# Kernel optimization log

Hardware: AMD Instinct MI355X
Metric: run time of the kernel (lower is better)

The kernel has to match this reference:

```python
import jax, jax.numpy as jnp
import numpy as np

N_NODES = 100000
N_EDGES = 3200000
IN_DIM, HID_DIM, OUT_DIM = 256, 128, 64


def setup_inputs() -> dict:
    key = jax.random.key(0)
    ks = jax.random.split(key, 8)
    x = jax.random.normal(ks[0], (N_NODES, IN_DIM), dtype=jnp.float32)
    edge_index = jax.random.randint(ks[1], (2, N_EDGES), 0, N_NODES, dtype=jnp.int64)
    s = 0.05
    return {
        "x": x,
        "edge_index": edge_index,
        "W1": jax.random.normal(ks[2], (IN_DIM, HID_DIM), dtype=jnp.float32) * s,
        "b1": jnp.zeros((HID_DIM,), dtype=jnp.float32),
        "W2": jax.random.normal(ks[3], (HID_DIM, HID_DIM), dtype=jnp.float32) * s,
        "b2": jnp.zeros((HID_DIM,), dtype=jnp.float32),
        "W3": jax.random.normal(ks[4], (HID_DIM, OUT_DIM), dtype=jnp.float32) * s,
        "b3": jnp.zeros((OUT_DIM,), dtype=jnp.float32),
    }


def _gcn_conv(x, src, dst, deg_inv_sqrt, W, b):
    """PyG GCNConv: D^-1/2 (A+I) D^-1/2 (X W) + b.
    src/dst already include self-loops; deg_inv_sqrt precomputed per node."""
    h = x @ W  # [N, F_out] - transform first (smaller message dim)
    norm = deg_inv_sqrt[src] * deg_inv_sqrt[dst]  # [E]
    msg = h[src] * norm[:, None]  # gather + scale
    out = jax.ops.segment_sum(msg, dst, num_segments=x.shape[0])  # scatter-add
    return out + b


def reference(x, edge_index, W1, b1, W2, b2, W3, b3):
    n = x.shape[0]
    loops = jnp.arange(n, dtype=edge_index.dtype)
    src = jnp.concatenate([edge_index[0], loops])
    dst = jnp.concatenate([edge_index[1], loops])
    # symmetric normalization degree over (A + I), counted on dst as in PyG
    deg = jax.ops.segment_sum(jnp.ones_like(dst, dtype=x.dtype), dst, num_segments=n)
    deg_inv_sqrt = jnp.where(deg > 0, jax.lax.rsqrt(deg), 0.0)

    h = _gcn_conv(x, src, dst, deg_inv_sqrt, W1, b1)
    h = jax.nn.relu(h)  # dropout in eval mode = identity
    h = _gcn_conv(h, src, dst, deg_inv_sqrt, W2, b2)
    h = jax.nn.relu(h)
    h = _gcn_conv(h, src, dst, deg_inv_sqrt, W3, b3)
    return h
```

## Files before the change

### kernel.cpp

```cpp
#include <hip/hip_runtime.h>
#include <hip/hip_fp16.h>

constexpr int IN_DIM  = 256;
constexpr int HID_DIM = 128;
constexpr int OUT_DIM = 64;

constexpr int NPB_SHIFT = 8;
constexpr int NPB   = 1 << NPB_SHIFT;
constexpr int NBMAX = 512;
constexpr int CHUNK = 4096;
constexpr int CAP_B = 12288;

typedef _Float16 half8 __attribute__((ext_vector_type(8)));
typedef float floatx4 __attribute__((ext_vector_type(4)));


__global__ __launch_bounds__(256) void k_hist(const int* __restrict__ dst, int E, int NB,
                                              int* __restrict__ bsize) {
  __shared__ int h[NBMAX];
  for (int i = threadIdx.x; i < NB; i += 256) h[i] = 0;
  __syncthreads();
  int e0 = blockIdx.x * CHUNK;
  int e1 = min(e0 + CHUNK, E);
  for (int e = e0 + threadIdx.x; e < e1; e += 256) {
    int d = __builtin_nontemporal_load(&dst[e]);
    atomicAdd(&h[d >> NPB_SHIFT], 1);
  }
  __syncthreads();
  for (int b = threadIdx.x; b < NB; b += 256) {
    int c = h[b];
    if (c) atomicAdd(&bsize[b], c);
  }
}

__global__ __launch_bounds__(512) void k_scanb(const int* __restrict__ bsize, int NB, int E,
                                               int* __restrict__ boff, int* __restrict__ gcur) {
  __shared__ int sh[NBMAX + 1];
  for (int i = threadIdx.x; i < NB; i += 512) sh[i] = bsize[i];
  __syncthreads();
  if (threadIdx.x == 0) {
    int run = 0;
    for (int b = 0; b < NB; b++) { int v = sh[b]; sh[b] = run; run += v; }
    sh[NB] = run;
  }
  __syncthreads();
  for (int i = threadIdx.x; i < NB; i += 512) { boff[i] = sh[i]; gcur[i] = sh[i]; }
  if (threadIdx.x == 0) boff[NB] = sh[NB];
}

__global__ __launch_bounds__(256) void k_binA(const int* __restrict__ src,
                                              const int* __restrict__ dst, int E, int NB,
                                              int* __restrict__ gcur,
                                              unsigned int* __restrict__ bin) {
  __shared__ unsigned int sbuf[CHUNK];
  __shared__ unsigned short sbb[CHUNK];
  __shared__ int h[NBMAX], lofs[NBMAX], wofs[NBMAX], hcur[NBMAX];
  for (int i = threadIdx.x; i < NB; i += 256) h[i] = 0;
  __syncthreads();
  int e0 = blockIdx.x * CHUNK;
  int e1 = min(e0 + CHUNK, E);
  for (int e = e0 + threadIdx.x; e < e1; e += 256) {
    int d = __builtin_nontemporal_load(&dst[e]);
    atomicAdd(&h[d >> NPB_SHIFT], 1);
  }
  __syncthreads();
  for (int b = threadIdx.x; b < NB; b += 256) {
    int c = h[b];
    if (c) wofs[b] = atomicAdd(&gcur[b], c);
  }
  if (threadIdx.x == 0) {
    int run = 0;
    for (int b = 0; b < NB; b++) { lofs[b] = run; run += h[b]; }
  }
  __syncthreads();
  for (int b = threadIdx.x; b < NB; b += 256) hcur[b] = lofs[b];
  __syncthreads();
  for (int e = e0 + threadIdx.x; e < e1; e += 256) {
    int d = dst[e];
    int s = src[e];
    int b = d >> NPB_SHIFT;
    int p = atomicAdd(&hcur[b], 1);
    sbuf[p] = ((unsigned int)(d & (NPB - 1)) << 24) | (unsigned int)s;
    sbb[p] = (unsigned short)b;
  }
  __syncthreads();
  int total = e1 - e0;
  for (int i = threadIdx.x; i < total; i += 256) {
    int b = sbb[i];
    bin[(size_t)wofs[b] + (i - lofs[b])] = sbuf[i];
  }
}

__global__ __launch_bounds__(256) void k_passB(const unsigned int* __restrict__ bin,
                                               const int* __restrict__ boff, int NB, int N, int E,
                                               int* __restrict__ rowptr, float* __restrict__ dis,
                                               int* __restrict__ col) {
  __shared__ unsigned int colbuf[CAP_B];
  __shared__ int lcnt[NPB], lofs2[NPB + 1], lpos[NPB];
  int b = blockIdx.x;
  int lo = b << NPB_SHIFT;
  int e0 = boff[b], e1 = boff[b + 1];
  int tot = e1 - e0;
  if (threadIdx.x < NPB) lcnt[threadIdx.x] = 0;
  __syncthreads();
  for (int i = threadIdx.x; i < tot; i += 256) {
    unsigned int v = bin[(size_t)e0 + i];
    atomicAdd(&lcnt[v >> 24], 1);
  }
  __syncthreads();
  if (threadIdx.x == 0) {
    int run = 0;
    for (int i = 0; i < NPB; i++) { lofs2[i] = run; run += lcnt[i]; }
    lofs2[NPB] = run;
  }
  __syncthreads();
  if (threadIdx.x < NPB) {
    int node = lo + threadIdx.x;
    if (node < N) {
      rowptr[node] = e0 + lofs2[threadIdx.x];
      dis[node] = rsqrtf((float)lcnt[threadIdx.x] + 1.0f);
    }
    lpos[threadIdx.x] = lofs2[threadIdx.x];
  }
  __syncthreads();
  for (int i = threadIdx.x; i < tot; i += 256) {
    unsigned int v = bin[(size_t)e0 + i];
    int idx = v >> 24;
    int p = atomicAdd(&lpos[idx], 1);
    unsigned int s = v & 0x00FFFFFFu;
    if (p < CAP_B) colbuf[p] = s;
    else col[(size_t)e0 + p] = (int)s;
  }
  __syncthreads();
  int cp = min(tot, CAP_B);
  for (int i = threadIdx.x; i < cp; i += 256)
    __builtin_nontemporal_store(colbuf[i], (unsigned int*)&col[(size_t)e0 + i]);
  if (b == 0 && threadIdx.x == 0) rowptr[N] = E;
}


template <int K, int N>
__device__ inline void packW_one(const float* __restrict__ W, _Float16* __restrict__ Wp,
                                 int idx) {
  int k = idx / N, n = idx % N;
  int ct = n >> 4, ks = k >> 5, q = (k >> 3) & 3, j = k & 7;
  int lane = (n & 15) + (q << 4);
  Wp[((((size_t)ct * (K / 32) + ks) * 64 + lane) << 3) + j] = (_Float16)W[idx];
}

__global__ __launch_bounds__(256) void k_packAll(const float* __restrict__ W1, _Float16* __restrict__ Wp1,
                                                 const float* __restrict__ W2, _Float16* __restrict__ Wp2,
                                                 const float* __restrict__ W3, _Float16* __restrict__ Wp3) {
  constexpr int S1 = IN_DIM * HID_DIM;
  constexpr int S2 = S1 + HID_DIM * HID_DIM;
  constexpr int S3 = S2 + HID_DIM * OUT_DIM;
  int idx = blockIdx.x * 256 + threadIdx.x;
  if (idx < S1) packW_one<IN_DIM, HID_DIM>(W1, Wp1, idx);
  else if (idx < S2) packW_one<HID_DIM, HID_DIM>(W2, Wp2, idx - S1);
  else if (idx < S3) packW_one<HID_DIM, OUT_DIM>(W3, Wp3, idx - S2);
}


template <int K, int N, typename AT>
__global__ __launch_bounds__(256) void k_gemm_mfma(const AT* __restrict__ A,
                                                   const _Float16* __restrict__ Wp,
                                                   const float* __restrict__ dis,
                                                   __half* __restrict__ out, int M) {
  constexpr int CT = N / 16;
  constexpr int KS = K / 32;
  constexpr int KH = (K * N * 2 > 32768) ? 2 : 1;
  constexpr int KSH = KS / KH;
  constexpr int NF4 = CT * KSH * 64;
  __shared__ float4 wlds[NF4];

  const int wave = threadIdx.x >> 6, lane = threadIdx.x & 63;
  const int q = lane >> 4, mlane = lane & 15;
  const int row0 = blockIdx.x * 64 + wave * 16;
  int arow = row0 + mlane;
  if (arow > M - 1) arow = M - 1;

  const float4* __restrict__ wsrc = (const float4*)Wp;

  floatx4 acc[CT];
#pragma unroll
  for (int c = 0; c < CT; c++) acc[c] = (floatx4){0.f, 0.f, 0.f, 0.f};

#pragma unroll
  for (int h = 0; h < KH; h++) {
    if (h) __syncthreads();
#pragma unroll
    for (int i = threadIdx.x; i < NF4; i += 256) {
      int c = i / (KSH * 64);
      int rem = i & (KSH * 64 - 1);
      wlds[i] = wsrc[(size_t)(c * KS + h * KSH) * 64 + rem];
    }
    __syncthreads();

#pragma unroll
    for (int ksl = 0; ksl < KSH; ksl++) {
      const int ks = h * KSH + ksl;
      half8 a;
      if constexpr (sizeof(AT) == 4) {
        const float* ap = &A[(size_t)arow * K + ks * 32 + q * 8];
        float4 f0 = *(const float4*)ap;
        float4 f1 = *(const float4*)(ap + 4);
        a[0] = (_Float16)f0.x; a[1] = (_Float16)f0.y;
        a[2] = (_Float16)f0.z; a[3] = (_Float16)f0.w;
        a[4] = (_Float16)f1.x; a[5] = (_Float16)f1.y;
        a[6] = (_Float16)f1.z; a[7] = (_Float16)f1.w;
      } else {
        a = *(const half8*)&A[(size_t)arow * K + ks * 32 + q * 8];
      }
#pragma unroll
      for (int c = 0; c < CT; c++) {
        half8 b = *(const half8*)&wlds[(c * KSH + ksl) * 64 + lane];
        acc[c] = __builtin_amdgcn_mfma_f32_16x16x32_f16(a, b, acc[c], 0, 0, 0);
      }
    }
  }

  float dv[4]; int orow[4];
#pragma unroll
  for (int r = 0; r < 4; r++) {
    orow[r] = row0 + q * 4 + r;
    dv[r] = (orow[r] < M) ? dis[orow[r]] : 0.f;
  }
#pragma unroll
  for (int c = 0; c < CT; c++) {
    int cl = c * 16 + mlane;
#pragma unroll
    for (int r = 0; r < 4; r++)
      if (orow[r] < M)
        out[(size_t)orow[r] * N + cl] = __float2half_rn(dv[r] * acc[c][r]);
  }
}


template <bool RELU>
__global__ __launch_bounds__(256) void k_agg128(const __half* __restrict__ g,
                                                const int* __restrict__ rowptr,
                                                const int* __restrict__ col,
                                                const float* __restrict__ dis,
                                                const float* __restrict__ bias,
                                                __half* __restrict__ out, int n) {
  const int lane = threadIdx.x & 63;
  const int r = lane >> 4;
  const int c = lane & 15;
  const int v = blockIdx.x * 4 + (threadIdx.x >> 6);
  if (v >= n) return;
  int p = rowptr[v], end = rowptr[v + 1];
  const float dv = dis[v];

  float acc[8];
#pragma unroll
  for (int i = 0; i < 8; i++) acc[i] = 0.f;
  if (r == 0) {
    half8 s = *(const half8*)&g[(size_t)v * 128 + c * 8];
#pragma unroll
    for (int i = 0; i < 8; i++) acc[i] += (float)s[i];
  }

  int rem = end - p;
  while (rem >= 8) {
    int u0 = __builtin_nontemporal_load(&col[p + r]);
    int u1 = __builtin_nontemporal_load(&col[p + 4 + r]);
    half8 t0 = *(const half8*)&g[(size_t)u0 * 128 + c * 8];
    half8 t1 = *(const half8*)&g[(size_t)u1 * 128 + c * 8];
#pragma unroll
    for (int i = 0; i < 8; i++) acc[i] += (float)t0[i];
#pragma unroll
    for (int i = 0; i < 8; i++) acc[i] += (float)t1[i];
    p += 8; rem -= 8;
  }
  if (rem >= 4) {
    int u0 = __builtin_nontemporal_load(&col[p + r]);
    half8 t0 = *(const half8*)&g[(size_t)u0 * 128 + c * 8];
#pragma unroll
    for (int i = 0; i < 8; i++) acc[i] += (float)t0[i];
    p += 4; rem -= 4;
  }
  if (rem > 0) {
    int rr = (r < rem) ? r : 0;
    int u0 = __builtin_nontemporal_load(&col[p + rr]);
    half8 t0 = *(const half8*)&g[(size_t)u0 * 128 + c * 8];
    float m = (r < rem) ? 1.f : 0.f;
#pragma unroll
    for (int i = 0; i < 8; i++) acc[i] = fmaf(m, (float)t0[i], acc[i]);
  }

#pragma unroll
  for (int i = 0; i < 8; i++) {
    acc[i] += __shfl_xor(acc[i], 16);
    acc[i] += __shfl_xor(acc[i], 32);
  }

  if (r == 0) {
    half8 h;
#pragma unroll
    for (int i = 0; i < 8; i++) {
      float o = fmaf(dv, acc[i], bias[c * 8 + i]);
      if (RELU) o = fmaxf(o, 0.f);
      h[i] = (_Float16)o;
    }
    *(half8*)&out[(size_t)v * 128 + c * 8] = h;
  }
}


__global__ __launch_bounds__(256) void k_agg64(const __half* __restrict__ g,
                                               const int* __restrict__ rowptr,
                                               const int* __restrict__ col,
                                               const float* __restrict__ dis,
                                               const float* __restrict__ bias,
                                               float* __restrict__ out, int n) {
  const int lane = threadIdx.x & 63;
  const int r = lane >> 3;
  const int c = lane & 7;
  const int v = blockIdx.x * 4 + (threadIdx.x >> 6);
  if (v >= n) return;
  int p = rowptr[v], end = rowptr[v + 1];
  const float dv = dis[v];

  float acc[8];
#pragma unroll
  for (int i = 0; i < 8; i++) acc[i] = 0.f;
  if (r == 0) {
    half8 s = *(const half8*)&g[(size_t)v * 64 + c * 8];
#pragma unroll
    for (int i = 0; i < 8; i++) acc[i] += (float)s[i];
  }

  int rem = end - p;
  while (rem >= 16) {
    int u0 = __builtin_nontemporal_load(&col[p + r]);
    int u1 = __builtin_nontemporal_load(&col[p + 8 + r]);
    half8 t0 = *(const half8*)&g[(size_t)u0 * 64 + c * 8];
    half8 t1 = *(const half8*)&g[(size_t)u1 * 64 + c * 8];
#pragma unroll
    for (int i = 0; i < 8; i++) acc[i] += (float)t0[i];
#pragma unroll
    for (int i = 0; i < 8; i++) acc[i] += (float)t1[i];
    p += 16; rem -= 16;
  }
  if (rem >= 8) {
    int u0 = __builtin_nontemporal_load(&col[p + r]);
    half8 t0 = *(const half8*)&g[(size_t)u0 * 64 + c * 8];
#pragma unroll
    for (int i = 0; i < 8; i++) acc[i] += (float)t0[i];
    p += 8; rem -= 8;
  }
  if (rem > 0) {
    int rr = (r < rem) ? r : 0;
    int u0 = __builtin_nontemporal_load(&col[p + rr]);
    half8 t0 = *(const half8*)&g[(size_t)u0 * 64 + c * 8];
    float m = (r < rem) ? 1.f : 0.f;
#pragma unroll
    for (int i = 0; i < 8; i++) acc[i] = fmaf(m, (float)t0[i], acc[i]);
  }

#pragma unroll
  for (int i = 0; i < 8; i++) {
    acc[i] += __shfl_xor(acc[i], 8);
    acc[i] += __shfl_xor(acc[i], 16);
    acc[i] += __shfl_xor(acc[i], 32);
  }

  if (r == 0) {
    float4 o0, o1;
    float ov[8];
#pragma unroll
    for (int i = 0; i < 8; i++) ov[i] = fmaf(dv, acc[i], bias[c * 8 + i]);
    o0.x = ov[0]; o0.y = ov[1]; o0.z = ov[2]; o0.w = ov[3];
    o1.x = ov[4]; o1.y = ov[5]; o1.z = ov[6]; o1.w = ov[7];
    *(float4*)&out[(size_t)v * 64 + c * 8]     = o0;
    *(float4*)&out[(size_t)v * 64 + c * 8 + 4] = o1;
  }
}


extern "C" void kernel_launch(void* const* d_in, const int* in_sizes, int n_in,
                              void* d_out, int out_size, void* d_ws, size_t ws_size,
                              hipStream_t stream) {
  const float* x  = (const float*)d_in[0];
  const int*   ei = (const int*)d_in[1];
  const float* W1 = (const float*)d_in[2];
  const float* b1 = (const float*)d_in[3];
  const float* W2 = (const float*)d_in[4];
  const float* b2 = (const float*)d_in[5];
  const float* W3 = (const float*)d_in[6];
  const float* b3 = (const float*)d_in[7];
  float* outp = (float*)d_out;

  const int N = in_sizes[0] / IN_DIM;
  const int E = in_sizes[1] / 2;
  const int* src = ei;
  const int* dst = ei + E;
  const int NB = (N + NPB - 1) >> NPB_SHIFT;

  char* w = (char*)d_ws;
  auto take = [&](size_t bytes) {
    char* r = w;
    w += (bytes + 255) & ~size_t(255);
    return r;
  };
  float*  dis    = (float*)take((size_t)N * 4);
  int*    rowptr = (int*)take((size_t)(N + 1) * 4);
  int*    bsize  = (int*)take((size_t)NB * 4);
  int*    boff   = (int*)take((size_t)(NB + 1) * 4);
  int*    gcur   = (int*)take((size_t)NB * 4);
  int*    col    = (int*)take((size_t)E * 4);
  unsigned int* bin = (unsigned int*)take((size_t)E * 4);
  _Float16* Wp1  = (_Float16*)take((size_t)IN_DIM * HID_DIM * 2);
  _Float16* Wp2  = (_Float16*)take((size_t)HID_DIM * HID_DIM * 2);
  _Float16* Wp3  = (_Float16*)take((size_t)HID_DIM * OUT_DIM * 2);
  __half* gbuf   = (__half*)take((size_t)N * 128 * 2);
  __half* bufH   = (__half*)take((size_t)N * 128 * 2);

  const int cb = (E + CHUNK - 1) / CHUNK;
  hipMemsetAsync(bsize, 0, (size_t)NB * 4, stream);
  hipLaunchKernelGGL(k_hist, dim3(cb), dim3(256), 0, stream, dst, E, NB, bsize);
  hipLaunchKernelGGL(k_scanb, dim3(1), dim3(512), 0, stream, bsize, NB, E, boff, gcur);
  hipLaunchKernelGGL(k_binA, dim3(cb), dim3(256), 0, stream, src, dst, E, NB, gcur, bin);
  hipLaunchKernelGGL(k_passB, dim3(NB), dim3(256), 0, stream, bin, boff, NB, N, E, rowptr, dis, col);

  hipLaunchKernelGGL(k_packAll, dim3((IN_DIM * HID_DIM + HID_DIM * HID_DIM + HID_DIM * OUT_DIM + 255) / 256),
                     dim3(256), 0, stream, W1, Wp1, W2, Wp2, W3, Wp3);

  const int gb = (N + 63) / 64;
  const int ab = (N + 3) / 4;
  hipLaunchKernelGGL((k_gemm_mfma<IN_DIM, HID_DIM, float>), dim3(gb), dim3(256), 0, stream, x, Wp1, dis, gbuf, N);
  hipLaunchKernelGGL((k_agg128<true>), dim3(ab), dim3(256), 0, stream, gbuf, rowptr, col, dis, b1, bufH, N);
  hipLaunchKernelGGL((k_gemm_mfma<HID_DIM, HID_DIM, __half>), dim3(gb), dim3(256), 0, stream, bufH, Wp2, dis, gbuf, N);
  hipLaunchKernelGGL((k_agg128<true>), dim3(ab), dim3(256), 0, stream, gbuf, rowptr, col, dis, b2, bufH, N);
  hipLaunchKernelGGL((k_gemm_mfma<HID_DIM, OUT_DIM, __half>), dim3(gb), dim3(256), 0, stream, bufH, Wp3, dis, gbuf, N);
  hipLaunchKernelGGL(k_agg64, dim3(ab), dim3(256), 0, stream, gbuf, rowptr, col, dis, b3, outp, N);
}
```

Before: 614.3 us.

## Batch neighbor index loads via wave shuffles and split 128-dim aggregation launches

```diff
diff --git a/kernel.cpp b/kernel.cpp
--- a/kernel.cpp
+++ b/kernel.cpp
@@ -242,11 +242,11 @@
                                                 const int* __restrict__ col,
                                                 const float* __restrict__ dis,
                                                 const float* __restrict__ bias,
-                                                __half* __restrict__ out, int n) {
+                                                __half* __restrict__ out, int n, int v0) {
   const int lane = threadIdx.x & 63;
   const int r = lane >> 4;
   const int c = lane & 15;
-  const int v = blockIdx.x * 4 + (threadIdx.x >> 6);
+  const int v = v0 + blockIdx.x * 4 + (threadIdx.x >> 6);
   if (v >= n) return;
   int p = rowptr[v], end = rowptr[v + 1];
   const float dv = dis[v];
@@ -260,32 +260,40 @@
     for (int i = 0; i < 8; i++) acc[i] += (float)s[i];
   }
 
-  int rem = end - p;
-  while (rem >= 8) {
-    int u0 = __builtin_nontemporal_load(&col[p + r]);
-    int u1 = __builtin_nontemporal_load(&col[p + 4 + r]);
-    half8 t0 = *(const half8*)&g[(size_t)u0 * 128 + c * 8];
-    half8 t1 = *(const half8*)&g[(size_t)u1 * 128 + c * 8];
-#pragma unroll
-    for (int i = 0; i < 8; i++) acc[i] += (float)t0[i];
-#pragma unroll
-    for (int i = 0; i < 8; i++) acc[i] += (float)t1[i];
-    p += 8; rem -= 8;
-  }
-  if (rem >= 4) {
-    int u0 = __builtin_nontemporal_load(&col[p + r]);
-    half8 t0 = *(const half8*)&g[(size_t)u0 * 128 + c * 8];
-#pragma unroll
-    for (int i = 0; i < 8; i++) acc[i] += (float)t0[i];
-    p += 4; rem -= 4;
-  }
-  if (rem > 0) {
-    int rr = (r < rem) ? r : 0;
-    int u0 = __builtin_nontemporal_load(&col[p + rr]);
-    half8 t0 = *(const half8*)&g[(size_t)u0 * 128 + c * 8];
-    float m = (r < rem) ? 1.f : 0.f;
-#pragma unroll
-    for (int i = 0; i < 8; i++) acc[i] = fmaf(m, (float)t0[i], acc[i]);
+  while (p < end) {
+    int navail = end - p;
+    if (navail > 64) navail = 64;
+    int cv = __builtin_nontemporal_load(&col[p + (lane < navail ? lane : 0)]);
+    int done = 0;
+    while (navail - done >= 8) {
+      int u0 = __shfl(cv, done + r);
+      int u1 = __shfl(cv, done + 4 + r);
+      half8 t0 = *(const half8*)&g[(size_t)u0 * 128 + c * 8];
+      half8 t1 = *(const half8*)&g[(size_t)u1 * 128 + c * 8];
+#pragma unroll
+      for (int i = 0; i < 8; i++) acc[i] += (float)t0[i];
+#pragma unroll
+      for (int i = 0; i < 8; i++) acc[i] += (float)t1[i];
+      done += 8;
+    }
+    int remn = navail - done;
+    if (remn > 0) {
+      int m0 = remn < 4 ? remn : 4;
+      int u0 = __shfl(cv, done + (r < m0 ? r : 0));
+      half8 t0 = *(const half8*)&g[(size_t)u0 * 128 + c * 8];
+      float k0 = (r < m0) ? 1.f : 0.f;
+#pragma unroll
+      for (int i = 0; i < 8; i++) acc[i] = fmaf(k0, (float)t0[i], acc[i]);
+      if (remn > 4) {
+        int m1 = remn - 4;
+        int u1 = __shfl(cv, done + 4 + (r < m1 ? r : 0));
+        half8 t1 = *(const half8*)&g[(size_t)u1 * 128 + c * 8];
+        float k1 = (r < m1) ? 1.f : 0.f;
+#pragma unroll
+        for (int i = 0; i < 8; i++) acc[i] = fmaf(k1, (float)t1[i], acc[i]);
+      }
+    }
+    p += navail;
   }
 
 #pragma unroll
@@ -330,32 +338,40 @@
     for (int i = 0; i < 8; i++) acc[i] += (float)s[i];
   }
 
-  int rem = end - p;
-  while (rem >= 16) {
-    int u0 = __builtin_nontemporal_load(&col[p + r]);
-    int u1 = __builtin_nontemporal_load(&col[p + 8 + r]);
-    half8 t0 = *(const half8*)&g[(size_t)u0 * 64 + c * 8];
-    half8 t1 = *(const half8*)&g[(size_t)u1 * 64 + c * 8];
-#pragma unroll
-    for (int i = 0; i < 8; i++) acc[i] += (float)t0[i];
-#pragma unroll
-    for (int i = 0; i < 8; i++) acc[i] += (float)t1[i];
-    p += 16; rem -= 16;
-  }
-  if (rem >= 8) {
-    int u0 = __builtin_nontemporal_load(&col[p + r]);
-    half8 t0 = *(const half8*)&g[(size_t)u0 * 64 + c * 8];
-#pragma unroll
-    for (int i = 0; i < 8; i++) acc[i] += (float)t0[i];
-    p += 8; rem -= 8;
-  }
-  if (rem > 0) {
-    int rr = (r < rem) ? r : 0;
-    int u0 = __builtin_nontemporal_load(&col[p + rr]);
-    half8 t0 = *(const half8*)&g[(size_t)u0 * 64 + c * 8];
-    float m = (r < rem) ? 1.f : 0.f;
-#pragma unroll
-    for (int i = 0; i < 8; i++) acc[i] = fmaf(m, (float)t0[i], acc[i]);
+  while (p < end) {
+    int navail = end - p;
+    if (navail > 64) navail = 64;
+    int cv = __builtin_nontemporal_load(&col[p + (lane < navail ? lane : 0)]);
+    int done = 0;
+    while (navail - done >= 16) {
+      int u0 = __shfl(cv, done + r);
+      int u1 = __shfl(cv, done + 8 + r);
+      half8 t0 = *(const half8*)&g[(size_t)u0 * 64 + c * 8];
+      half8 t1 = *(const half8*)&g[(size_t)u1 * 64 + c * 8];
+#pragma unroll
+      for (int i = 0; i < 8; i++) acc[i] += (float)t0[i];
+#pragma unroll
+      for (int i = 0; i < 8; i++) acc[i] += (float)t1[i];
+      done += 16;
+    }
+    int remn = navail - done;
+    if (remn > 0) {
+      int m0 = remn < 8 ? remn : 8;
+      int u0 = __shfl(cv, done + (r < m0 ? r : 0));
+      half8 t0 = *(const half8*)&g[(size_t)u0 * 64 + c * 8];
+      float k0 = (r < m0) ? 1.f : 0.f;
+#pragma unroll
+      for (int i = 0; i < 8; i++) acc[i] = fmaf(k0, (float)t0[i], acc[i]);
+      if (remn > 8) {
+        int m1 = remn - 8;
+        int u1 = __shfl(cv, done + 8 + (r < m1 ? r : 0));
+        half8 t1 = *(const half8*)&g[(size_t)u1 * 64 + c * 8];
+        float k1 = (r < m1) ? 1.f : 0.f;
+#pragma unroll
+        for (int i = 0; i < 8; i++) acc[i] = fmaf(k1, (float)t1[i], acc[i]);
+      }
+    }
+    p += navail;
   }
 
 #pragma unroll
@@ -428,10 +444,15 @@
 
   const int gb = (N + 63) / 64;
   const int ab = (N + 3) / 4;
+  const int nh = (N + 1) / 2;
+  const int ab1 = (nh + 3) / 4;
+  const int ab2 = (N - nh + 3) / 4;
   hipLaunchKernelGGL((k_gemm_mfma<IN_DIM, HID_DIM, float>), dim3(gb), dim3(256), 0, stream, x, Wp1, dis, gbuf, N);
-  hipLaunchKernelGGL((k_agg128<true>), dim3(ab), dim3(256), 0, stream, gbuf, rowptr, col, dis, b1, bufH, N);
+  hipLaunchKernelGGL((k_agg128<true>), dim3(ab1), dim3(256), 0, stream, gbuf, rowptr, col, dis, b1, bufH, N, 0);
+  hipLaunchKernelGGL((k_agg128<true>), dim3(ab2), dim3(256), 0, stream, gbuf, rowptr, col, dis, b1, bufH, N, nh);
   hipLaunchKernelGGL((k_gemm_mfma<HID_DIM, HID_DIM, __half>), dim3(gb), dim3(256), 0, stream, bufH, Wp2, dis, gbuf, N);
-  hipLaunchKernelGGL((k_agg128<true>), dim3(ab), dim3(256), 0, stream, gbuf, rowptr, col, dis, b2, bufH, N);
+  hipLaunchKernelGGL((k_agg128<true>), dim3(ab1), dim3(256), 0, stream, gbuf, rowptr, col, dis, b2, bufH, N, 0);
+  hipLaunchKernelGGL((k_agg128<true>), dim3(ab2), dim3(256), 0, stream, gbuf, rowptr, col, dis, b2, bufH, N, nh);
   hipLaunchKernelGGL((k_gemm_mfma<HID_DIM, OUT_DIM, __half>), dim3(gb), dim3(256), 0, stream, bufH, Wp3, dis, gbuf, N);
   hipLaunchKernelGGL(k_agg64, dim3(ab), dim3(256), 0, stream, gbuf, rowptr, col, dis, b3, outp, N);
 }
```

After: 595.3 us. -3.1%, faster.
